# Performance work log

Measured on AMD Instinct MI355X. Metric: run time of the kernel, lower is better.

Reference implementation:

```python
import jax, jax.numpy as jnp
import numpy as np

B, V, C = 256, 50, 40
VOCAB, D, H, NH, T = 10000, 256, 256, 8, 1000


def setup_inputs():
    key = jax.random.key(0)
    ks = jax.random.split(key, 24)
    f = lambda k, shape, s=0.05: jax.random.normal(k, shape, jnp.float32) * s
    # nn.Embedding(vocab_size+1, d_model, padding_idx=-1): last row is the padding row (zeros)
    emb = f(ks[0], (VOCAB + 1, D), 0.1).at[VOCAB].set(0.0)
    return dict(
        input_seqs=jax.random.randint(ks[1], (B, V, C), 0, VOCAB),
        seq_time_step=jax.random.uniform(ks[2], (B, V), jnp.float32, 0.0, 365.0),
        diffusion_time_t=jax.random.randint(ks[3], (B,), 0, T),
        normal_noise=jax.random.normal(ks[4], (B, V, D), jnp.float32),
        predicted_noise=jax.random.normal(ks[5], (B, V, D), jnp.float32),
        emb=emb,
        betas=jnp.asarray(np.linspace(1e-4, 0.02, T, dtype=np.float32)),
        tl_w=f(ks[6], (64, 1), 0.5), tl_b=f(ks[7], (64,), 0.1),
        tu_w=f(ks[8], (D, 64)), tu_b=f(ks[9], (D,), 0.01),
        in_proj_w=f(ks[10], (3 * D, D)), in_proj_b=f(ks[11], (3 * D,), 0.01),
        out_proj_w=f(ks[12], (D, D)), out_proj_b=f(ks[13], (D,), 0.01),
        w_ih=f(ks[14], (4 * H, D)), w_hh=f(ks[15], (4 * H, H)),
        b_ih=f(ks[16], (4 * H,), 0.01), b_hh=f(ks[17], (4 * H,), 0.01),
        c1_w=f(ks[18], (4 * H, H)), c1_b=f(ks[19], (4 * H,), 0.01),
        c2_w=f(ks[20], (4 * H, 4 * H)), c2_b=f(ks[21], (4 * H,), 0.01),
        co_w=f(ks[22], (2, 4 * H)), co_b=f(ks[23], (2,), 0.01),
    )


def _mha(q, kv, wi, bi, wo, bo):
    # torch MultiheadAttention on 2-D inputs -> unbatched; 'sequence length' = batch dim B
    hd = D // NH
    qp = (q @ wi[:D].T + bi[:D]).reshape(-1, NH, hd)
    kp = (kv @ wi[D:2 * D].T + bi[D:2 * D]).reshape(-1, NH, hd)
    vp = (kv @ wi[2 * D:].T + bi[2 * D:]).reshape(-1, NH, hd)
    s = jnp.einsum('qhd,khd->hqk', qp, kp) * (hd ** -0.5)
    o = jnp.einsum('hqk,khd->qhd', jax.nn.softmax(s, -1), vp).reshape(-1, D)
    return o @ wo.T + bo


def _lstm_final(seq, w_ih, w_hh, b_ih, b_hh):
    # unbatched nn.LSTM over the batch axis (length B). The original's try-branch always
    # raises (seq_h squeezed to 1-D), so the zero-init except-branch runs every visit.
    xg = seq @ w_ih.T + (b_ih + b_hh)  # [B, 4H]
    def step(carry, x):
        h, c = carry
        i, fg, g, o = jnp.split(x + h @ w_hh.T, 4)
        c = jax.nn.sigmoid(fg) * c + jax.nn.sigmoid(i) * jnp.tanh(g)
        h = jax.nn.sigmoid(o) * jnp.tanh(c)
        return (h, c), None
    z = jnp.zeros((H,), seq.dtype)
    (h, _), _ = jax.lax.scan(step, (z, z), xg)
    return h  # [H]


def _classify(h, w1, b1, w2, b2, wo, bo):
    h = jax.nn.relu(h @ w1.T + b1)
    h = jax.nn.relu(h @ w2.T + b2)
    return jax.nn.softmax(h @ wo.T + bo, -1)


def reference(input_seqs, seq_time_step, diffusion_time_t, normal_noise, predicted_noise,
              emb, betas, tl_w, tl_b, tu_w, tu_b, in_proj_w, in_proj_b, out_proj_w,
              out_proj_b, w_ih, w_hh, b_ih, b_hh, c1_w, c1_b, c2_w, c2_b, co_w, co_b):
    tt = seq_time_step[..., None] / 180.0
    tenc = (1.0 - jnp.tanh((tt @ tl_w.T + tl_b) ** 2)) @ tu_w.T + tu_b  # [B,V,D]
    ve = jax.nn.relu(emb[input_seqs]).sum(-2) + tenc                     # [B,V,D]
    alpha = jnp.cumprod(1.0 - betas)[diffusion_time_t][:, None, None]
    ven = ve * jnp.sqrt(alpha) + normal_noise * jnp.sqrt(1.0 - alpha)
    gen1 = ve + (ven - predicted_noise)
    # gen2 recurrence: row i = MHA(row i-1, gen1[:,i], gen1[:,i]); row -1 is the
    # vocab_size-filled initial tensor (valid negative index, try never fails).
    def att_step(prev, kv):
        out = _mha(prev, kv, in_proj_w, in_proj_b, out_proj_w, out_proj_b)
        return out, out
    _, gen2 = jax.lax.scan(att_step, jnp.full((B, D), float(VOCAB), ve.dtype),
                           gen1.transpose(1, 0, 2))                    # [V,B,D]
    lstm = lambda s: _lstm_final(s, w_ih, w_hh, b_ih, b_hh)
    hv = jax.vmap(lstm)(ve.transpose(1, 0, 2))  # [V,H]
    hg = jax.vmap(lstm)(gen2)                   # [V,H]
    res = jnp.broadcast_to(_classify(hv, c1_w, c1_b, c2_w, c2_b, co_w, co_b)[None], (B, V, 2))
    resg = jnp.broadcast_to(_classify(hg, c1_w, c1_b, c2_w, c2_b, co_w, co_b)[None], (B, V, 2))
    return (res, resg, res[:, -1], resg[:, -1], normal_noise, predicted_noise)
```

## Files before the change

kernel.cpp:

```cpp
#include <hip/hip_runtime.h>

#define BB 256
#define VV 50
#define CC 40
#define DD 256
#define HH 256
#define NHH 8
#define TT 1000

typedef unsigned short u16;
typedef unsigned int u32;
typedef _Float16 h2v __attribute__((ext_vector_type(2)));

__device__ __forceinline__ float blf(u16 x){ union{u32 u; float f;} z; z.u=(u32)x<<16; return z.f; }
__device__ __forceinline__ float ld(const void* p, long i, int f){
  if(f) return ((const float*)p)[i];
  return blf(((const u16*)p)[i]);
}
__device__ __forceinline__ u32 packh2(float a, float b){
  union { h2v h; u32 u; } z;
  z.h = h2v{(_Float16)a, (_Float16)b};
  return z.u;
}
__device__ __forceinline__ float fdot2(u32 a, u32 b, float c){
#if __has_builtin(__builtin_amdgcn_fdot2)
  union { u32 u; h2v h; } x, y; x.u=a; y.u=b;
  return __builtin_amdgcn_fdot2(x.h, y.h, c, false);
#else
  union { u32 u; _Float16 h[2]; } x, y; x.u=a; y.u=b;
  return c + (float)x.h[0]*(float)y.h[0] + (float)x.h[1]*(float)y.h[1];
#endif
}
__device__ __forceinline__ float sigm(float x){ return 1.f/(1.f+__expf(-x)); }
__device__ __forceinline__ float tanh_fast(float x){ return 1.f - 2.f/(__expf(2.f*x)+1.f); }

__global__ void k_flag(const void* betas, int* flag){
  if(threadIdx.x==0) flag[0] = (((const u32*)betas)[0] == 0x38D1B717u) ? 1 : 0;
}

__global__ void k_prep(const void* betas, const int* fl, float* sqa, float* s1a){
  __shared__ float sp[256];
  int t = threadIdx.x;
  int f = fl[0];
  float om[4]; float p = 1.f;
  #pragma unroll
  for(int k=0;k<4;k++){ int i=t*4+k; float be=(i<TT)?ld(betas,i,f):0.f; om[k]=1.f-be; p*=om[k]; }
  sp[t]=p; __syncthreads();
  for(int off=1; off<256; off<<=1){
    float x = (t>=off) ? sp[t-off]*sp[t] : sp[t];
    __syncthreads(); sp[t]=x; __syncthreads();
  }
  float c = (t>0)? sp[t-1] : 1.f;
  #pragma unroll
  for(int k=0;k<4;k++){
    c *= om[k]; int i=t*4+k;
    if(i<TT){ sqa[i]=sqrtf(c); s1a[i]=sqrtf(fmaxf(1.f-c,0.f)); }
  }
}

__global__ void k_packT(const void* src, float* dst, int N, int K, long elemoff, const int* fl){
  int i = blockIdx.x*256 + threadIdx.x;
  int tot = N*(K>>2);
  if(i>=tot) return;
  int f = fl[0];
  int d4 = i / N, j = i - d4*N;
  long o = elemoff + (long)j*K + (d4<<2);
  float4 r; r.x=ld(src,o,f); r.y=ld(src,o+1,f); r.z=ld(src,o+2,f); r.w=ld(src,o+3,f);
  ((float4*)dst)[i] = r;
}

__global__ void k_packQO(const void* src, u32* dst, long elemoff, const int* fl){
  int i = blockIdx.x*256 + threadIdx.x;
  if(i >= 32768) return;
  int f = fl[0];
  int c2 = i >> 8, j = i & 255;
  float a = ld(src, elemoff + (long)j*256 + 2*c2,     f);
  float b = ld(src, elemoff + (long)j*256 + 2*c2 + 1, f);
  dst[(c2>>2)*1024 + j*4 + (c2&3)] = packh2(a,b);
}

__global__ void k_packW(const void* src, u32* whhB, u32* whhC, const int* fl){
  int i = blockIdx.x*256 + threadIdx.x;
  if(i >= 131072) return;
  int f = fl[0];
  int c2 = i >> 10, row = i & 1023;
  float a = ld(src, (long)row*256 + 2*c2,     f);
  float b = ld(src, (long)row*256 + 2*c2 + 1, f);
  u32 v = packh2(a,b);
  if(c2 < 96) whhB[c2*1024 + row] = v;
  else { int c = c2-96; whhC[(c>>2)*4096 + row*4 + (c&3)] = v; }
}

__global__ void k_ve_gen1(const int* seqs, const void* sts, const int* dt,
    const void* nn, const void* pn, const void* emb, const void* tl_w, const void* tl_b,
    const float* tu4, const void* tu_b, const float* sqa, const float* s1a, const int* fl,
    float* ve, float* gen1){
  int bv = blockIdx.x; int b = bv / VV;
  int t = threadIdx.x;
  int f = fl[0];
  __shared__ float4 f4[16];
  __shared__ int idx[CC];
  float tt = ld(sts,bv,f) * (1.f/180.f);
  if(t<64){ float x = tt*ld(tl_w,t,f) + ld(tl_b,t,f); ((float*)f4)[t] = 1.f - tanhf(x*x); }
  if(t<CC) idx[t] = seqs[bv*CC+t];
  __syncthreads();
  float acc = ld(tu_b,t,f);
  const float4* tu = (const float4*)tu4;
  #pragma unroll
  for(int d4=0; d4<16; d4++){
    float4 w = tu[d4*DD + t];
    float4 fv = f4[d4];
    acc += fv.x*w.x+fv.y*w.y+fv.z*w.z+fv.w*w.w;
  }
  float s=0.f;
  for(int c=0;c<CC;c++){ float e = ld(emb,(long)idx[c]*DD + t,f); s += fmaxf(e,0.f); }
  float vev = s + acc;
  ve[bv*DD+t] = vev;
  int tb = dt[b];
  float sa=sqa[tb], s1=s1a[tb];
  gen1[bv*DD+t] = vev*(1.f+sa) + ld(nn,(long)bv*DD+t,f)*s1 - ld(pn,(long)bv*DD+t,f);
}

__global__ void k_copy(const void* nn, const void* pn, const int* fl, float* out){
  int i = blockIdx.x*256 + threadIdx.x;
  int f = fl[0];
  const int n = BB*VV*DD;
  if(i<n){ out[52224+i]=ld(nn,i,f); out[52224+n+i]=ld(pn,i,f); }
}

__global__ void k_kvproj(const float* gen1, const float* wk4, const float* wv4,
                         const void* bi, const int* fl, float* kpT, u32* vp){
  int g = blockIdx.x; int v = g>>4; int b0 = (g&15)<<4;
  int t = threadIdx.x;
  int f = fl[0];
  __shared__ float4 x4[16][64];
  for(int r=0;r<16;r++) ((float*)x4[r])[t] = gen1[((b0+r)*VV + v)*DD + t];
  __syncthreads();
  float ak[16], av[16];
  float bk = ld(bi,DD+t,f), bvv = ld(bi,2*DD+t,f);
  #pragma unroll
  for(int r=0;r<16;r++){ ak[r]=bk; av[r]=bvv; }
  const float4* wk = (const float4*)wk4;
  const float4* wv = (const float4*)wv4;
  for(int d4=0; d4<64; d4++){
    float4 k4 = wk[d4*DD+t], v4 = wv[d4*DD+t];
    #pragma unroll
    for(int r=0;r<16;r++){
      float4 xv = x4[r][d4];
      ak[r] += xv.x*k4.x + xv.y*k4.y + xv.z*k4.z + xv.w*k4.w;
      av[r] += xv.x*v4.x + xv.y*v4.y + xv.z*v4.z + xv.w*v4.w;
    }
  }
  float* kdst = kpT + (v*DD + t)*BB + b0;
  #pragma unroll
  for(int r=0;r<16;r++) kdst[r] = ak[r];
  #pragma unroll
  for(int i2=0;i2<8;i2++){
    int k2 = (b0>>1) + i2;
    vp[(size_t)v*32768 + (k2>>2)*1024 + t*4 + (k2&3)] = packh2(av[2*i2], av[2*i2+1]);
  }
}

__global__ __launch_bounds__(256) void k_mha_all(const float* kpT, const u32* vp,
    const u32* wqp, const u32* wop, const void* ipb, const void* opb, const int* fl,
    float* gen2){
  int i = blockIdx.x, t = threadIdx.x;
  int f = fl[0];
  __shared__ u32 xp[128];
  __shared__ float q[256];
  __shared__ float s[NHH][257];
  __shared__ u32 sp[NHH][128];
  __shared__ u32 op[128];
  __shared__ float mh[NHH], rs[NHH];
  float bq = ld(ipb, t, f);
  float bo = ld(opb, t, f);
  if(t < 128) xp[t] = packh2(10000.f, 10000.f);
  __syncthreads();
  const uint4* xp4 = (const uint4*)xp;
  const uint4* op4 = (const uint4*)op;
  const uint4* wq4p = (const uint4*)wqp;
  const uint4* wo4p = (const uint4*)wop;
  int hg = t>>5, ln = t&31;
  for(int v=0; v<VV; v++){
    {
      float acc = bq;
      #pragma unroll 8
      for(int c8=0;c8<32;c8++){
        uint4 xx = xp4[c8];
        uint4 ww = wq4p[c8*256 + t];
        acc = fdot2(xx.x, ww.x, acc); acc = fdot2(xx.y, ww.y, acc);
        acc = fdot2(xx.z, ww.z, acc); acc = fdot2(xx.w, ww.w, acc);
      }
      q[t] = acc;
    }
    __syncthreads();
    {
      const float* kb = kpT + (size_t)v*BB*DD;
      #pragma unroll
      for(int h=0; h<NHH; h++){
        float acc=0.f;
        #pragma unroll
        for(int d=0; d<32; d++) acc += q[h*32+d]*kb[(h*32+d)*BB + t];
        s[h][t] = acc*0.1767766952966369f;
      }
    }
    __syncthreads();
    float m=-3.0e38f;
    for(int k=ln;k<BB;k+=32) m=fmaxf(m, s[hg][k]);
    for(int off=16;off;off>>=1) m=fmaxf(m, __shfl_down(m,off,32));
    if(ln==0) mh[hg]=m;
    __syncthreads();
    #pragma unroll
    for(int h=0;h<NHH;h++) s[h][t]=__expf(s[h][t]-mh[h]);
    __syncthreads();
    float sm=0.f;
    for(int k=ln;k<BB;k+=32) sm += s[hg][k];
    for(int off=16;off;off>>=1) sm += __shfl_down(sm,off,32);
    if(ln==0) rs[hg]=1.f/sm;
    #pragma unroll
    for(int m2=t; m2<1024; m2+=256){
      int h = m2>>7, k2 = m2&127;
      sp[h][k2] = packh2(s[h][2*k2], s[h][2*k2+1]);
    }
    __syncthreads();
    {
      const uint4* vb = (const uint4*)(vp + (size_t)v*32768);
      const uint4* spv = (const uint4*)sp[hg];
      float acc = 0.f;
      #pragma unroll 8
      for(int k8=0;k8<32;k8++){
        uint4 pv = spv[k8];
        uint4 vv = vb[k8*256 + t];
        acc = fdot2(pv.x, vv.x, acc); acc = fdot2(pv.y, vv.y, acc);
        acc = fdot2(pv.z, vv.z, acc); acc = fdot2(pv.w, vv.w, acc);
      }
      float o = acc * rs[hg];
      float oo = __shfl_xor(o, 1, 64);
      if((t&1)==0) op[t>>1] = packh2(o, oo);
    }
    __syncthreads();
    {
      float acc = bo;
      #pragma unroll 8
      for(int c8=0;c8<32;c8++){
        uint4 xx = op4[c8];
        uint4 ww = wo4p[c8*256 + t];
        acc = fdot2(xx.x, ww.x, acc); acc = fdot2(xx.y, ww.y, acc);
        acc = fdot2(xx.z, ww.z, acc); acc = fdot2(xx.w, ww.w, acc);
      }
      gen2[((size_t)v*BB+i)*DD + t] = acc;
      float ax = __shfl_xor(acc, 1, 64);
      if((t&1)==0) xp[t>>1] = packh2(acc, ax);
    }
    __syncthreads();
  }
}

__global__ __launch_bounds__(256, 2) void k_xg(const float* inp, int is_ve, const float* wih4,
                     const void* b_ih, const void* b_hh, const int* fl, u16* xg){
  int g = blockIdx.x; int v=g>>4; int b0=(g&15)<<4;
  int t = threadIdx.x;
  int f = fl[0];
  __shared__ float4 x4[16][64];
  for(int r=0;r<16;r++){
    int b = b0+r;
    const float* src = is_ve ? (inp + (b*VV+v)*DD) : (inp + (v*BB+b)*DD);
    ((float*)x4[r])[t] = src[t];
  }
  __syncthreads();
  float acc[4][16];
  #pragma unroll
  for(int js=0;js<4;js++){
    float bsum = ld(b_ih,js*256+t,f) + ld(b_hh,js*256+t,f);
    #pragma unroll
    for(int r=0;r<16;r++) acc[js][r]=bsum;
  }
  const float4* wf = (const float4*)wih4;
  #pragma unroll 2
  for(int d4=0; d4<64; d4++){
    float4 w[4];
    #pragma unroll
    for(int js=0;js<4;js++) w[js] = wf[d4*1024 + js*256 + t];
    #pragma unroll
    for(int r=0;r<16;r++){
      float4 xv = x4[r][d4];
      #pragma unroll
      for(int js=0;js<4;js++)
        acc[js][r] += xv.x*w[js].x+xv.y*w[js].y+xv.z*w[js].z+xv.w*w[js].w;
    }
  }
  for(int r=0;r<16;r++)
    #pragma unroll
    for(int js=0;js<4;js++){
      union { _Float16 h; u16 u; } z;
      z.h = (_Float16)acc[js][r];
      xg[(size_t)(v*BB + b0 + r)*1024 + js*256 + t] = z.u;
    }
}

__global__ __attribute__((amdgpu_flat_work_group_size(512,512)))
__attribute__((amdgpu_waves_per_eu(2,2)))
void k_lstm3(const u16* xgA, const u16* xgB,
    const u32* whhB, const u32* whhC, float* hfin){
  int b = blockIdx.x, j = threadIdx.x;
  const u16* xgv = (b < VV) ? (xgA + (size_t)b*BB*1024) : (xgB + (size_t)(b-VV)*BB*1024);
  __shared__ __align__(16) u32 wcl[32768];
  __shared__ __align__(16) u32 hp[128];
  __shared__ __align__(16) float gacc[1024];
  u32 w0[96], w1[96];
  #pragma unroll
  for(int c2=0;c2<96;c2++){
    w0[c2] = whhB[c2*1024 + j];
    w1[c2] = whhB[c2*1024 + 512 + j];
  }
  {
    const uint4* src = (const uint4*)whhC;
    uint4* dst = (uint4*)wcl;
    #pragma unroll
    for(int i=0;i<16;i++) dst[i*512 + j] = src[i*512 + j];
  }
  if(j < 128) hp[j] = 0u;
  float c0 = 0.f, h_t = 0.f;
  u16 nx0 = xgv[j], nx1 = xgv[512 + j];
  __syncthreads();
  const uint4* hp4 = (const uint4*)hp;
  const uint4* wcl4 = (const uint4*)wcl;
  for(int s=0; s<BB; s++){
    asm volatile("" ::: "memory");
    float a0  = (float)(*(const _Float16*)&nx0);
    float a1  = (float)(*(const _Float16*)&nx1);
    float a0b = 0.f, a1b = 0.f;
    if(s+1 < BB){ nx0 = xgv[(s+1)*1024 + j]; nx1 = xgv[(s+1)*1024 + 512 + j]; }
    #pragma unroll
    for(int c8=0;c8<24;c8++){
      uint4 hh = hp4[c8];
      a0  = fdot2(hh.x, w0[4*c8+0], a0 );
      a0b = fdot2(hh.y, w0[4*c8+1], a0b);
      a0  = fdot2(hh.z, w0[4*c8+2], a0 );
      a0b = fdot2(hh.w, w0[4*c8+3], a0b);
      a1  = fdot2(hh.x, w1[4*c8+0], a1 );
      a1b = fdot2(hh.y, w1[4*c8+1], a1b);
      a1  = fdot2(hh.z, w1[4*c8+2], a1 );
      a1b = fdot2(hh.w, w1[4*c8+3], a1b);
    }
    #pragma unroll
    for(int c4=0;c4<8;c4++){
      uint4 s0 = wcl4[c4*1024 + j];
      uint4 s1 = wcl4[c4*1024 + 512 + j];
      uint4 hh = hp4[24 + c4];
      a0  = fdot2(hh.x, s0.x, a0 ); a0b = fdot2(hh.y, s0.y, a0b);
      a0  = fdot2(hh.z, s0.z, a0 ); a0b = fdot2(hh.w, s0.w, a0b);
      a1  = fdot2(hh.x, s1.x, a1 ); a1b = fdot2(hh.y, s1.y, a1b);
      a1  = fdot2(hh.z, s1.z, a1 ); a1b = fdot2(hh.w, s1.w, a1b);
    }
    gacc[j] = a0 + a0b;
    gacc[512 + j] = a1 + a1b;
    __syncthreads();
    if(j < 256){
      float ai = gacc[j], af = gacc[256+j], ag = gacc[512+j], ao = gacc[768+j];
      float ig = sigm(ai), fg = sigm(af), og = sigm(ao);
      float gg = tanh_fast(ag);
      c0 = fg*c0 + ig*gg;
      h_t = og*tanh_fast(c0);
      float ho = __shfl_xor(h_t, 1, 64);
      if((j&1)==0) hp[j>>1] = packh2(h_t, ho);
    }
    __syncthreads();
  }
  if(j < 256) hfin[b*HH + j] = h_t;
}

__global__ void k_cls(const float* hfin, const float* c14, const void* c1b,
                      const float* c24, const void* c2b, const void* cow, const void* cob,
                      const int* fl, float* cls){
  int blk = blockIdx.x;
  int t = threadIdx.x;
  int f = fl[0];
  __shared__ float4 h4[64];
  __shared__ float4 h14[256];
  __shared__ float4 h24[256];
  __shared__ float red0[4], red1[4];
  ((float*)h4)[t] = hfin[blk*HH + t];
  __syncthreads();
  {
    float a[4];
    #pragma unroll
    for(int js=0;js<4;js++) a[js]=ld(c1b,js*256+t,f);
    const float4* wf = (const float4*)c14;
    for(int d4=0; d4<64; d4++){
      float4 hv = h4[d4];
      #pragma unroll
      for(int js=0;js<4;js++){
        float4 w = wf[d4*1024 + js*256+t];
        a[js] += hv.x*w.x+hv.y*w.y+hv.z*w.z+hv.w*w.w;
      }
    }
    #pragma unroll
    for(int js=0;js<4;js++) ((float*)h14)[js*256+t] = fmaxf(a[js],0.f);
  }
  __syncthreads();
  {
    float a[4];
    #pragma unroll
    for(int js=0;js<4;js++) a[js]=ld(c2b,js*256+t,f);
    const float4* wf = (const float4*)c24;
    for(int d4=0; d4<256; d4++){
      float4 hv = h14[d4];
      #pragma unroll
      for(int js=0;js<4;js++){
        float4 w = wf[d4*1024 + js*256+t];
        a[js] += hv.x*w.x+hv.y*w.y+hv.z*w.z+hv.w*w.w;
      }
    }
    #pragma unroll
    for(int js=0;js<4;js++) ((float*)h24)[js*256+t] = fmaxf(a[js],0.f);
  }
  __syncthreads();
  float p0=0.f,p1=0.f;
  #pragma unroll
  for(int js=0;js<4;js++){
    int j=js*256+t;
    float hv=((float*)h24)[j];
    p0 += hv*ld(cow,j,f);
    p1 += hv*ld(cow,1024+j,f);
  }
  for(int off=32;off;off>>=1){ p0+=__shfl_down(p0,off,64); p1+=__shfl_down(p1,off,64); }
  if((t&63)==0){ red0[t>>6]=p0; red1[t>>6]=p1; }
  __syncthreads();
  if(t==0){
    float l0 = ld(cob,0,f) + red0[0]+red0[1]+red0[2]+red0[3];
    float l1 = ld(cob,1,f) + red1[0]+red1[1]+red1[2]+red1[3];
    float mm = fmaxf(l0,l1);
    float e0=__expf(l0-mm), e1=__expf(l1-mm);
    float inv = 1.f/(e0+e1);
    cls[blk*2] = e0*inv; cls[blk*2+1] = e1*inv;
  }
}

__global__ void k_out(const float* cls, float* out){
  int i = blockIdx.x*256 + threadIdx.x;
  if(i < BB*VV*2){
    int v = (i>>1) % VV, k = i&1;
    out[i] = cls[v*2+k];
    out[BB*VV*2 + i] = cls[(VV+v)*2+k];
  }
  if(i < BB*2){
    int k=i&1;
    out[2*BB*VV*2 + i]        = cls[(VV-1)*2+k];
    out[2*BB*VV*2 + BB*2 + i] = cls[(2*VV-1)*2+k];
  }
}

extern "C" void kernel_launch(void* const* d_in, const int* in_sizes, int n_in,
                              void* d_out, int out_size, void* d_ws, size_t ws_size,
                              hipStream_t stream){
  const int* seqs = (const int*)d_in[0];
  const void* sts  = d_in[1];
  const int* dt   = (const int*)d_in[2];
  const void* nn   = d_in[3];
  const void* pn   = d_in[4];
  const void* emb  = d_in[5];
  const void* betas= d_in[6];
  const void* tl_w = d_in[7];
  const void* tl_b = d_in[8];
  const void* tu_w = d_in[9];
  const void* tu_b = d_in[10];
  const void* ipw  = d_in[11];
  const void* ipb  = d_in[12];
  const void* opw  = d_in[13];
  const void* opb  = d_in[14];
  const void* wih  = d_in[15];
  const void* whh  = d_in[16];
  const void* bih  = d_in[17];
  const void* bhh  = d_in[18];
  const void* c1w  = d_in[19];
  const void* c1b  = d_in[20];
  const void* c2w  = d_in[21];
  const void* c2b  = d_in[22];
  const void* cow  = d_in[23];
  const void* cob  = d_in[24];

  char* base = (char*)d_ws;
  float* wk4  = (float*)(base + 0);
  float* wv4  = (float*)(base + 262144);
  u32*   wqp  = (u32*)(base + 524288);
  u32*   wop  = (u32*)(base + 655360);
  float* wih4 = (float*)(base + 786432);
  u32*   whhB = (u32*)(base + 1835008);
  u32*   whhC = (u32*)(base + 2228224);
  float* c14  = (float*)(base + 2359296);
  float* c24  = (float*)(base + 3407872);
  float* tu4  = (float*)(base + 7602176);
  float* sqa  = (float*)(base + 7667712);
  float* s1a  = (float*)(base + 7671808);
  float* hfin = (float*)(base + 7675904);
  float* cls  = (float*)(base + 7778304);
  int*   flag = (int*)(base + 7779328);
  float* ve   = (float*)(base + 7783424);
  float* g12  = (float*)(base + 20890624);
  char*  arena= base + 33997824;
  float* kpT  = (float*)(arena);
  u32*   vp   = (u32*)(arena + 13107200);
  u16*   xgA  = (u16*)(arena);
  u16*   xgB  = (u16*)(arena + 26214400);
  float* out  = (float*)d_out;

  k_flag<<<1,64,0,stream>>>(betas, flag);
  k_prep<<<1,256,0,stream>>>(betas, flag, sqa, s1a);
  k_packT<<<64,256,0,stream>>>(ipw,  wk4, 256, 256, 65536L,  flag);
  k_packT<<<64,256,0,stream>>>(ipw,  wv4, 256, 256, 131072L, flag);
  k_packQO<<<128,256,0,stream>>>(ipw, wqp, 0, flag);
  k_packQO<<<128,256,0,stream>>>(opw, wop, 0, flag);
  k_packT<<<256,256,0,stream>>>(wih, wih4,1024, 256, 0, flag);
  k_packW<<<512,256,0,stream>>>(whh, whhB, whhC, flag);
  k_packT<<<256,256,0,stream>>>(c1w, c14, 1024, 256, 0, flag);
  k_packT<<<1024,256,0,stream>>>(c2w,c24, 1024,1024, 0, flag);
  k_packT<<<16,256,0,stream>>>(tu_w, tu4, 256, 64, 0, flag);

  k_ve_gen1<<<BB*VV,256,0,stream>>>(seqs,sts,dt,nn,pn,emb,tl_w,tl_b,tu4,tu_b,sqa,s1a,flag,ve,g12);
  k_copy<<<(BB*VV*DD+255)/256,256,0,stream>>>(nn,pn,flag,out);

  k_kvproj<<<VV*16,256,0,stream>>>(g12, wk4, wv4, ipb, flag, kpT, vp);
  k_mha_all<<<BB,256,0,stream>>>(kpT, vp, wqp, wop, ipb, opb, flag, g12);

  k_xg<<<VV*16,256,0,stream>>>(ve,  1, wih4, bih, bhh, flag, xgA);
  k_xg<<<VV*16,256,0,stream>>>(g12, 0, wih4, bih, bhh, flag, xgB);
  k_lstm3<<<100,512,0,stream>>>(xgA, xgB, whhB, whhC, hfin);

  k_cls<<<2*VV,256,0,stream>>>(hfin, c14, c1b, c24, c2b, cow, cob, flag, cls);
  k_out<<<100,256,0,stream>>>(cls, out);
}
```

Measured before the change: 1.868 ms.

## Split LSTM recurrent matvec across K quarters with shared-memory partial sums

The LSTM recurrence kernel is repartitioned. Before, each thread owned two full gate rows over all 256 hidden inputs. Now each thread owns 8 gate rows over a 64-element K-quarter, so it reads a quarter as many h broadcasts from LDS and keeps weights in 192 registers plus LDS. Partial sums for the four quarters are written to LDS and reduced by 256 threads, which also load the xg inputs for that step directly instead of prefetching them. The weight packing kernel is rewritten to match the new layout. This costs more LDS traffic for partials and a 4-way reduction, and drops the xg prefetch, which puts global-load latency inside the serial loop.

```diff
diff --git a/kernel.cpp b/kernel.cpp
--- a/kernel.cpp
+++ b/kernel.cpp
@@ -79,16 +79,24 @@
   dst[(c2>>2)*1024 + j*4 + (c2&3)] = packh2(a,b);
 }
 
-__global__ void k_packW(const void* src, u32* whhB, u32* whhC, const int* fl){
+__global__ void k_packW2(const void* src, u32* whhR, u32* wclQ, const int* fl){
   int i = blockIdx.x*256 + threadIdx.x;
   if(i >= 131072) return;
   int f = fl[0];
-  int c2 = i >> 10, row = i & 1023;
-  float a = ld(src, (long)row*256 + 2*c2,     f);
-  float b = ld(src, (long)row*256 + 2*c2 + 1, f);
+  int row = i >> 7, cp = i & 127;
+  float a = ld(src, (long)row*256 + 2*cp,     f);
+  float b = ld(src, (long)row*256 + 2*cp + 1, f);
   u32 v = packh2(a,b);
-  if(c2 < 96) whhB[c2*1024 + row] = v;
-  else { int c = c2-96; whhC[(c>>2)*4096 + row*4 + (c&3)] = v; }
+  int q = cp >> 5, pp = cp & 31;
+  int rb = row & 127, m = row >> 7;
+  int j = q*128 + rb;
+  if(pp < 24){
+    int idx = m*24 + pp;
+    whhR[(idx>>2)*2048 + j*4 + (idx&3)] = v;
+  } else {
+    int h = (pp-24) >> 2, e = (pp-24) & 3;
+    wclQ[((m*2+h)*512 + j)*4 + e] = v;
+  }
 }
 
 __global__ void k_ve_gen1(const int* seqs, const void* sts, const int* dt,
@@ -301,63 +309,78 @@
 __global__ __attribute__((amdgpu_flat_work_group_size(512,512)))
 __attribute__((amdgpu_waves_per_eu(2,2)))
 void k_lstm3(const u16* xgA, const u16* xgB,
-    const u32* whhB, const u32* whhC, float* hfin){
+    const u32* whhR, const u32* wclQ, float* hfin){
   int b = blockIdx.x, j = threadIdx.x;
+  int q = j >> 7, rb = j & 127;
   const u16* xgv = (b < VV) ? (xgA + (size_t)b*BB*1024) : (xgB + (size_t)(b-VV)*BB*1024);
   __shared__ __align__(16) u32 wcl[32768];
+  __shared__ __align__(16) float pacc[4][1024];
   __shared__ __align__(16) u32 hp[128];
-  __shared__ __align__(16) float gacc[1024];
-  u32 w0[96], w1[96];
-  #pragma unroll
-  for(int c2=0;c2<96;c2++){
-    w0[c2] = whhB[c2*1024 + j];
-    w1[c2] = whhB[c2*1024 + 512 + j];
-  }
+  u32 w[192];
+  { const uint4* wr4 = (const uint4*)whhR;
+    #pragma unroll
+    for(int i4=0;i4<48;i4++){
+      uint4 v = wr4[i4*512 + j];
+      w[i4*4+0]=v.x; w[i4*4+1]=v.y; w[i4*4+2]=v.z; w[i4*4+3]=v.w;
+    } }
   {
-    const uint4* src = (const uint4*)whhC;
+    const uint4* src = (const uint4*)wclQ;
     uint4* dst = (uint4*)wcl;
     #pragma unroll
     for(int i=0;i<16;i++) dst[i*512 + j] = src[i*512 + j];
   }
   if(j < 128) hp[j] = 0u;
   float c0 = 0.f, h_t = 0.f;
-  u16 nx0 = xgv[j], nx1 = xgv[512 + j];
   __syncthreads();
   const uint4* hp4 = (const uint4*)hp;
   const uint4* wcl4 = (const uint4*)wcl;
   for(int s=0; s<BB; s++){
     asm volatile("" ::: "memory");
-    float a0  = (float)(*(const _Float16*)&nx0);
-    float a1  = (float)(*(const _Float16*)&nx1);
-    float a0b = 0.f, a1b = 0.f;
-    if(s+1 < BB){ nx0 = xgv[(s+1)*1024 + j]; nx1 = xgv[(s+1)*1024 + 512 + j]; }
-    #pragma unroll
-    for(int c8=0;c8<24;c8++){
-      uint4 hh = hp4[c8];
-      a0  = fdot2(hh.x, w0[4*c8+0], a0 );
-      a0b = fdot2(hh.y, w0[4*c8+1], a0b);
-      a0  = fdot2(hh.z, w0[4*c8+2], a0 );
-      a0b = fdot2(hh.w, w0[4*c8+3], a0b);
-      a1  = fdot2(hh.x, w1[4*c8+0], a1 );
-      a1b = fdot2(hh.y, w1[4*c8+1], a1b);
-      a1  = fdot2(hh.z, w1[4*c8+2], a1 );
-      a1b = fdot2(hh.w, w1[4*c8+3], a1b);
-    }
-    #pragma unroll
-    for(int c4=0;c4<8;c4++){
-      uint4 s0 = wcl4[c4*1024 + j];
-      uint4 s1 = wcl4[c4*1024 + 512 + j];
-      uint4 hh = hp4[24 + c4];
-      a0  = fdot2(hh.x, s0.x, a0 ); a0b = fdot2(hh.y, s0.y, a0b);
-      a0  = fdot2(hh.z, s0.z, a0 ); a0b = fdot2(hh.w, s0.w, a0b);
-      a1  = fdot2(hh.x, s1.x, a1 ); a1b = fdot2(hh.y, s1.y, a1b);
-      a1  = fdot2(hh.z, s1.z, a1 ); a1b = fdot2(hh.w, s1.w, a1b);
-    }
-    gacc[j] = a0 + a0b;
-    gacc[512 + j] = a1 + a1b;
-    __syncthreads();
+    u16 nx0=0,nx1=0,nx2=0,nx3=0;
     if(j < 256){
-      float ai = gacc[j], af = gacc[256+j], ag = gacc[512+j], ao = gacc[768+j];
+      nx0 = xgv[s*1024 +       j];
+      nx1 = xgv[s*1024 + 256 + j];
+      nx2 = xgv[s*1024 + 512 + j];
+      nx3 = xgv[s*1024 + 768 + j];
+    }
+    float acc[8];
+    #pragma unroll
+    for(int m=0;m<8;m++) acc[m]=0.f;
+    #pragma unroll
+    for(int i=0;i<6;i++){
+      uint4 hh = hp4[q*8 + i];
+      #pragma unroll
+      for(int m=0;m<8;m++){
+        acc[m] = fdot2(hh.x, w[m*24 + i*4+0], acc[m]);
+        acc[m] = fdot2(hh.y, w[m*24 + i*4+1], acc[m]);
+        acc[m] = fdot2(hh.z, w[m*24 + i*4+2], acc[m]);
+        acc[m] = fdot2(hh.w, w[m*24 + i*4+3], acc[m]);
+      }
+    }
+    #pragma unroll
+    for(int h=0;h<2;h++){
+      uint4 hh = hp4[q*8 + 6 + h];
+      #pragma unroll
+      for(int m=0;m<8;m++){
+        uint4 s4 = wcl4[(m*2+h)*512 + j];
+        acc[m] = fdot2(hh.x, s4.x, acc[m]);
+        acc[m] = fdot2(hh.y, s4.y, acc[m]);
+        acc[m] = fdot2(hh.z, s4.z, acc[m]);
+        acc[m] = fdot2(hh.w, s4.w, acc[m]);
+      }
+    }
+    #pragma unroll
+    for(int m=0;m<8;m++) pacc[q][m*128 + rb] = acc[m];
+    __syncthreads();
+    if(j < 256){
+      float a0 = pacc[0][      j] + pacc[1][      j] + pacc[2][      j] + pacc[3][      j];
+      float a1 = pacc[0][256 + j] + pacc[1][256 + j] + pacc[2][256 + j] + pacc[3][256 + j];
+      float a2 = pacc[0][512 + j] + pacc[1][512 + j] + pacc[2][512 + j] + pacc[3][512 + j];
+      float a3 = pacc[0][768 + j] + pacc[1][768 + j] + pacc[2][768 + j] + pacc[3][768 + j];
+      float ai = a0 + (float)(*(const _Float16*)&nx0);
+      float af = a1 + (float)(*(const _Float16*)&nx1);
+      float ag = a2 + (float)(*(const _Float16*)&nx2);
+      float ao = a3 + (float)(*(const _Float16*)&nx3);
       float ig = sigm(ai), fg = sigm(af), og = sigm(ao);
       float gg = tanh_fast(ag);
       c0 = fg*c0 + ig*gg;
@@ -486,8 +509,8 @@
   u32*   wqp  = (u32*)(base + 524288);
   u32*   wop  = (u32*)(base + 655360);
   float* wih4 = (float*)(base + 786432);
-  u32*   whhB = (u32*)(base + 1835008);
-  u32*   whhC = (u32*)(base + 2228224);
+  u32*   whhR = (u32*)(base + 1835008);
+  u32*   wclQ = (u32*)(base + 2228224);
   float* c14  = (float*)(base + 2359296);
   float* c24  = (float*)(base + 3407872);
   float* tu4  = (float*)(base + 7602176);
@@ -512,7 +535,7 @@
   k_packQO<<<128,256,0,stream>>>(ipw, wqp, 0, flag);
   k_packQO<<<128,256,0,stream>>>(opw, wop, 0, flag);
   k_packT<<<256,256,0,stream>>>(wih, wih4,1024, 256, 0, flag);
-  k_packW<<<512,256,0,stream>>>(whh, whhB, whhC, flag);
+  k_packW2<<<512,256,0,stream>>>(whh, whhR, wclQ, flag);
   k_packT<<<256,256,0,stream>>>(c1w, c14, 1024, 256, 0, flag);
   k_packT<<<1024,256,0,stream>>>(c2w,c24, 1024,1024, 0, flag);
   k_packT<<<16,256,0,stream>>>(tu_w, tu4, 256, 64, 0, flag);
@@ -525,7 +548,7 @@
 
   k_xg<<<VV*16,256,0,stream>>>(ve,  1, wih4, bih, bhh, flag, xgA);
   k_xg<<<VV*16,256,0,stream>>>(g12, 0, wih4, bih, bhh, flag, xgB);
-  k_lstm3<<<100,512,0,stream>>>(xgA, xgB, whhB, whhC, hfin);
+  k_lstm3<<<100,512,0,stream>>>(xgA, xgB, whhR, wclQ, hfin);
 
   k_cls<<<2*VV,256,0,stream>>>(hfin, c14, c1b, c24, c2b, cow, cob, flag, cls);
   k_out<<<100,256,0,stream>>>(cls, out);
```

New measurement: 1.787 ms. 1.05x faster.
